# Kernel optimization log

Measured on AMD Instinct MI355X. Metric: run time of the kernel, lower is better.

## Reference

```python
import jax, jax.numpy as jnp
import numpy as np


def setup_inputs() -> dict:
    key = jax.random.key(0)
    kx, kw, kt, ks, kd, km = jax.random.split(key, 6)
    B, N, E, H, D = 1, 100000, 3200000, 8, 64
    X = jax.random.normal(kx, (B, N, H, D), dtype=jnp.float32)
    # glorot_uniform-like init for [D, H, 1]
    limit = (6.0 / (D + H)) ** 0.5
    attn_kernel = jax.random.uniform(kw, (D, H, 1), dtype=jnp.float32, minval=-limit, maxval=limit)
    targets = jax.random.randint(kt, (B, E), 0, N)
    sources = jax.random.randint(ks, (B, E), 0, N)
    degree = jax.random.uniform(kd, (B, N), dtype=jnp.float32)
    # tf.nn.dropout(x, 0.5): keep w.p. 0.5, scale kept by 1/0.5 = 2
    drop_mask = (jax.random.uniform(km, (B, E, H)) < 0.5).astype(jnp.float32) * 2.0
    return {"X": X, "attn_kernel": attn_kernel, "targets": targets,
            "sources": sources, "degree": degree, "drop_mask": drop_mask, "N": N}


def reference(X, attn_kernel, targets, sources, degree, drop_mask, N):
    # X: [B, N, H, D]; attn_kernel: [D, H, 1]; targets/sources: [B, E]
    B, _, H, D = X.shape
    E = targets.shape[1]
    W = attn_kernel[:, :, 0]                          # [D, H]
    attn = jnp.einsum('bnhd,dh->bnh', X, W)           # per-node scalar per head
    # gather to edges (tf.gather batch_dims=1): [B, E, H]
    e = jnp.take_along_axis(attn, sources[..., None], axis=1)
    e = jnp.tanh(e)
    # TF unsorted_segment_max with rank-2 ids pools over (batch, edge) jointly
    ids = targets.reshape(B * E)
    ef = e.reshape(B * E, H)
    m = jax.ops.segment_max(ef, ids, num_segments=N)  # [N, H]
    ef = jnp.exp(ef - m[ids])
    s = jax.ops.segment_max(ef, ids, num_segments=N) + 1e-9  # NOTE: max, not sum (faithful)
    ef = ef / s[ids]
    out = ef.reshape(B, E, H) * drop_mask
    return out[..., None]                             # [B, E, H, 1]
```

## Files before the change

kernel.cpp:

```cpp
#include <hip/hip_runtime.h>
#include <stdint.h>

#define HD 8
#define DD 64

typedef float  vf4 __attribute__((ext_vector_type(4)));
typedef unsigned vu4 __attribute__((ext_vector_type(4)));

__device__ __forceinline__ unsigned fmap(float f) {
    unsigned u = __float_as_uint(f);
    return u ^ (unsigned)(((int)u >> 31) | 0x80000000);
}
__device__ __forceinline__ float funmap(unsigned u) {
    u ^= ((int)u < 0) ? 0x80000000u : 0xFFFFFFFFu;
    return __uint_as_float(u);
}
#define FMAP_NEG_INF 0x007FFFFFu

__device__ __forceinline__ unsigned pack_bf16_rne(float a, float b) {
    unsigned ua = __float_as_uint(a); ua += 0x7FFF + ((ua >> 16) & 1);
    unsigned ub = __float_as_uint(b); ub += 0x7FFF + ((ub >> 16) & 1);
    return (ua >> 16) | (ub & 0xFFFF0000u);
}
__device__ __forceinline__ float bf_lo(unsigned u) { return __uint_as_float(u << 16); }
__device__ __forceinline__ float bf_hi(unsigned u) { return __uint_as_float(u & 0xFFFF0000u); }

__global__ __launch_bounds__(256) void attn_tanh_kernel(
    const float* __restrict__ X, const float* __restrict__ Wk,
    unsigned* __restrict__ t_pk, uint2* __restrict__ m_init, int N)
{
    __shared__ float Ws[DD * HD];
    int tid = threadIdx.x;
    for (int i = tid; i < DD * HD; i += 256) Ws[i] = Wk[i];
    __syncthreads();

    int wave = tid >> 6, lane = tid & 63;
    int n0 = (blockIdx.x * 4 + wave) * 2;
    if (n0 >= N) return;
    bool two = (n0 + 1 < N);

    const vf4* Xa = (const vf4*)X + (size_t)n0 * 128;
    vf4 z = {0.f, 0.f, 0.f, 0.f};
    vf4 xv0 = __builtin_nontemporal_load(Xa + lane);
    vf4 xv1 = __builtin_nontemporal_load(Xa + 64 + lane);
    vf4 xv2 = two ? __builtin_nontemporal_load(Xa + 128 + lane) : z;
    vf4 xv3 = two ? __builtin_nontemporal_load(Xa + 192 + lane) : z;

    int h0 = lane >> 4, d0 = (lane & 15) << 2;
    int h1 = 4 + h0;
    float w00 = Ws[(d0 + 0) * HD + h0], w01 = Ws[(d0 + 1) * HD + h0],
          w02 = Ws[(d0 + 2) * HD + h0], w03 = Ws[(d0 + 3) * HD + h0];
    float w10 = Ws[(d0 + 0) * HD + h1], w11 = Ws[(d0 + 1) * HD + h1],
          w12 = Ws[(d0 + 2) * HD + h1], w13 = Ws[(d0 + 3) * HD + h1];

    float p0 = xv0.x * w00 + xv0.y * w01 + xv0.z * w02 + xv0.w * w03;
    float p1 = xv1.x * w10 + xv1.y * w11 + xv1.z * w12 + xv1.w * w13;
    float p2 = xv2.x * w00 + xv2.y * w01 + xv2.z * w02 + xv2.w * w03;
    float p3 = xv3.x * w10 + xv3.y * w11 + xv3.z * w12 + xv3.w * w13;

    for (int off = 8; off; off >>= 1) {
        p0 += __shfl_xor(p0, off);
        p1 += __shfl_xor(p1, off);
        p2 += __shfl_xor(p2, off);
        p3 += __shfl_xor(p3, off);
    }
    if ((lane & 15) == 0) {
        int g = lane >> 4;
        t_pk[(size_t)n0 * 4 + g] = pack_bf16_rne(tanhf(p0), tanhf(p1));
        m_init[(size_t)n0 * 4 + g] = make_uint2(FMAP_NEG_INF, FMAP_NEG_INF);
        if (two) {
            t_pk[(size_t)(n0 + 1) * 4 + g] = pack_bf16_rne(tanhf(p2), tanhf(p3));
            m_init[(size_t)(n0 + 1) * 4 + g] = make_uint2(FMAP_NEG_INF, FMAP_NEG_INF);
        }
    }
}

__global__ __launch_bounds__(256) void seg_max_kernel(
    const int* __restrict__ sources, const int* __restrict__ targets,
    const uint4* __restrict__ t_pk4, unsigned* __restrict__ m_u, int E)
{
    int e = blockIdx.x * 256 + threadIdx.x;
    if (e >= E) return;
    int s  = __builtin_nontemporal_load(sources + e);
    int tg = __builtin_nontemporal_load(targets + e);
    uint4 tv = t_pk4[s];
    unsigned* mp = m_u + (size_t)tg * HD;
    const uint4* m4 = (const uint4*)mp;
    uint4 c0 = m4[0];
    uint4 c1 = m4[1];
    unsigned f;
    f = fmap(bf_lo(tv.x)); if (f > c0.x) atomicMax(mp + 0, f);
    f = fmap(bf_hi(tv.x)); if (f > c0.y) atomicMax(mp + 1, f);
    f = fmap(bf_lo(tv.y)); if (f > c0.z) atomicMax(mp + 2, f);
    f = fmap(bf_hi(tv.y)); if (f > c0.w) atomicMax(mp + 3, f);
    f = fmap(bf_lo(tv.z)); if (f > c1.x) atomicMax(mp + 4, f);
    f = fmap(bf_hi(tv.z)); if (f > c1.y) atomicMax(mp + 5, f);
    f = fmap(bf_lo(tv.w)); if (f > c1.z) atomicMax(mp + 6, f);
    f = fmap(bf_hi(tv.w)); if (f > c1.w) atomicMax(mp + 7, f);
}

__global__ __launch_bounds__(256) void pack_m_kernel(
    const unsigned* __restrict__ m_u, uint4* __restrict__ m_pk, int N)
{
    int n = blockIdx.x * 256 + threadIdx.x;
    if (n >= N) return;
    const uint4* mu4 = (const uint4*)m_u + (size_t)n * 2;
    uint4 c0 = mu4[0];
    uint4 c1 = mu4[1];
    uint4 o;
    o.x = (__float_as_uint(funmap(c0.x)) >> 16) | (__float_as_uint(funmap(c0.y)) & 0xFFFF0000u);
    o.y = (__float_as_uint(funmap(c0.z)) >> 16) | (__float_as_uint(funmap(c0.w)) & 0xFFFF0000u);
    o.z = (__float_as_uint(funmap(c1.x)) >> 16) | (__float_as_uint(funmap(c1.y)) & 0xFFFF0000u);
    o.w = (__float_as_uint(funmap(c1.z)) >> 16) | (__float_as_uint(funmap(c1.w)) & 0xFFFF0000u);
    m_pk[n] = o;
}

__global__ __launch_bounds__(256) void finalize_kernel(
    const int* __restrict__ sources, const int* __restrict__ targets,
    const uint4* __restrict__ t_pk4, const uint4* __restrict__ m_pk,
    const float* __restrict__ dm, float* __restrict__ out, int E)
{
    int e = blockIdx.x * 256 + threadIdx.x;
    if (e >= E) return;
    int s  = __builtin_nontemporal_load(sources + e);
    int tg = __builtin_nontemporal_load(targets + e);
    uint4 tv = t_pk4[s];
    uint4 mv = m_pk[tg];
    const vf4* dm4 = (const vf4*)dm;
    vf4 d0 = __builtin_nontemporal_load(dm4 + (size_t)e * 2);
    vf4 d1 = __builtin_nontemporal_load(dm4 + (size_t)e * 2 + 1);
    vf4 o0, o1;
    o0.x = expf(bf_lo(tv.x) - bf_lo(mv.x)) * d0.x;
    o0.y = expf(bf_lo(tv.y) - bf_lo(mv.y)) * d0.y;
    o0.z = expf(bf_lo(tv.z) - bf_lo(mv.z)) * d0.z;
    o0.w = expf(bf_lo(tv.w) - bf_lo(mv.w)) * d0.w;
    o1.x = expf(bf_hi(tv.x) - bf_hi(mv.x)) * d1.x;
    o1.y = expf(bf_hi(tv.y) - bf_hi(mv.y)) * d1.y;
    o1.z = expf(bf_hi(tv.z) - bf_hi(mv.z)) * d1.z;
    o1.w = expf(bf_hi(tv.w) - bf_hi(mv.w)) * d1.w;
    vf4* out4 = (vf4*)out;
    __builtin_nontemporal_store(o0, out4 + (size_t)e * 2);
    __builtin_nontemporal_store(o1, out4 + (size_t)e * 2 + 1);
}

extern "C" void kernel_launch(void* const* d_in, const int* in_sizes, int n_in,
                              void* d_out, int out_size, void* d_ws, size_t ws_size,
                              hipStream_t stream)
{
    const float* X       = (const float*)d_in[0];
    const float* Wk      = (const float*)d_in[1];
    const int*   targets = (const int*)d_in[2];
    const int*   sources = (const int*)d_in[3];
    const float* dm      = (const float*)d_in[5];

    int E = in_sizes[2];
    int N = in_sizes[4];

    unsigned* t_pk = (unsigned*)d_ws;
    unsigned* m_u  = (unsigned*)d_ws + (size_t)N * 4;
    uint4*    m_pk = (uint4*)((unsigned*)d_ws + (size_t)N * 12);

    float* out = (float*)d_out;

    int blocksA = (N + 7) / 8;
    attn_tanh_kernel<<<blocksA, 256, 0, stream>>>(X, Wk, t_pk, (uint2*)m_u, N);

    int blocksE = (E + 255) / 256;
    seg_max_kernel<<<blocksE, 256, 0, stream>>>(sources, targets, (const uint4*)t_pk, m_u, E);

    int blocksN = (N + 255) / 256;
    pack_m_kernel<<<blocksN, 256, 0, stream>>>(m_u, m_pk, N);

    finalize_kernel<<<blocksE, 256, 0, stream>>>(sources, targets, (const uint4*)t_pk, m_pk, dm, out, E);
}
```

Before: 640.9 us.

## Replace per-edge atomicMax segment-max with bucketed edge lists and wave reduction

Per-edge segment max is restructured so each edge does one atomicAdd on a per-target counter and stores its source index into a fixed-capacity per-target bucket. Edges past the bucket capacity fall back to atomicMax. A new per-node kernel reduces each bucket with one wave using shuffles and writes packed bf16 maxima, replacing the pack kernel. This trades up to eight contended atomics per edge for one atomicAdd plus a scattered index write, but adds a large list buffer and an extra gather pass over t_pk. Counter zeroing is folded into the attention kernel, and the old path stays as a fallback when workspace is too small.

```diff
diff --git a/kernel.cpp b/kernel.cpp
--- a/kernel.cpp
+++ b/kernel.cpp
@@ -3,9 +3,9 @@
 
 #define HD 8
 #define DD 64
+#define CAP 64
 
 typedef float  vf4 __attribute__((ext_vector_type(4)));
-typedef unsigned vu4 __attribute__((ext_vector_type(4)));
 
 __device__ __forceinline__ unsigned fmap(float f) {
     unsigned u = __float_as_uint(f);
@@ -27,11 +27,16 @@
 
 __global__ __launch_bounds__(256) void attn_tanh_kernel(
     const float* __restrict__ X, const float* __restrict__ Wk,
-    unsigned* __restrict__ t_pk, uint2* __restrict__ m_init, int N)
+    unsigned* __restrict__ t_pk, uint2* __restrict__ m_init,
+    unsigned* __restrict__ cnt, int N)
 {
     __shared__ float Ws[DD * HD];
     int tid = threadIdx.x;
     for (int i = tid; i < DD * HD; i += 256) Ws[i] = Wk[i];
+
+    int gid = blockIdx.x * 256 + tid;
+    if (cnt != nullptr && gid < N) cnt[gid] = 0;
+
     __syncthreads();
 
     int wave = tid >> 6, lane = tid & 63;
@@ -74,6 +79,84 @@
         }
     }
 }
+
+__global__ __launch_bounds__(256) void scatter_kernel(
+    const int* __restrict__ sources, const int* __restrict__ targets,
+    unsigned* __restrict__ cnt, unsigned* __restrict__ lst,
+    const uint4* __restrict__ t_pk4, unsigned* __restrict__ m_u, int E)
+{
+    int e = blockIdx.x * 256 + threadIdx.x;
+    if (e >= E) return;
+    int s  = __builtin_nontemporal_load(sources + e);
+    int tg = __builtin_nontemporal_load(targets + e);
+    unsigned pos = atomicAdd(cnt + tg, 1u);
+    if (pos < CAP) {
+        lst[(size_t)tg * CAP + pos] = (unsigned)s;
+    } else {
+        uint4 tv = t_pk4[s];
+        unsigned* mp = m_u + (size_t)tg * HD;
+        atomicMax(mp + 0, fmap(bf_lo(tv.x)));
+        atomicMax(mp + 1, fmap(bf_hi(tv.x)));
+        atomicMax(mp + 2, fmap(bf_lo(tv.y)));
+        atomicMax(mp + 3, fmap(bf_hi(tv.y)));
+        atomicMax(mp + 4, fmap(bf_lo(tv.z)));
+        atomicMax(mp + 5, fmap(bf_hi(tv.z)));
+        atomicMax(mp + 6, fmap(bf_lo(tv.w)));
+        atomicMax(mp + 7, fmap(bf_hi(tv.w)));
+    }
+}
+
+__global__ __launch_bounds__(256) void gather_max_kernel(
+    const unsigned* __restrict__ cnt, const unsigned* __restrict__ lst,
+    const uint4* __restrict__ t_pk4, const unsigned* __restrict__ m_u,
+    uint4* __restrict__ m_pk, int N)
+{
+    int wave = threadIdx.x >> 6, lane = threadIdx.x & 63;
+    int n = blockIdx.x * 4 + wave;
+    if (n >= N) return;
+
+    unsigned c = cnt[n];
+    if (c > CAP) c = CAP;
+
+    float v0 = -INFINITY, v1 = -INFINITY, v2 = -INFINITY, v3 = -INFINITY,
+          v4 = -INFINITY, v5 = -INFINITY, v6 = -INFINITY, v7 = -INFINITY;
+    if ((unsigned)lane < c) {
+        unsigned s = lst[(size_t)n * CAP + lane];
+        uint4 tv = t_pk4[s];
+        v0 = bf_lo(tv.x); v1 = bf_hi(tv.x);
+        v2 = bf_lo(tv.y); v3 = bf_hi(tv.y);
+        v4 = bf_lo(tv.z); v5 = bf_hi(tv.z);
+        v6 = bf_lo(tv.w); v7 = bf_hi(tv.w);
+    }
+    for (int off = 32; off; off >>= 1) {
+        v0 = fmaxf(v0, __shfl_xor(v0, off));
+        v1 = fmaxf(v1, __shfl_xor(v1, off));
+        v2 = fmaxf(v2, __shfl_xor(v2, off));
+        v3 = fmaxf(v3, __shfl_xor(v3, off));
+        v4 = fmaxf(v4, __shfl_xor(v4, off));
+        v5 = fmaxf(v5, __shfl_xor(v5, off));
+        v6 = fmaxf(v6, __shfl_xor(v6, off));
+        v7 = fmaxf(v7, __shfl_xor(v7, off));
+    }
+    if (lane == 0) {
+        const unsigned* mu = m_u + (size_t)n * HD;
+        v0 = fmaxf(v0, funmap(mu[0]));
+        v1 = fmaxf(v1, funmap(mu[1]));
+        v2 = fmaxf(v2, funmap(mu[2]));
+        v3 = fmaxf(v3, funmap(mu[3]));
+        v4 = fmaxf(v4, funmap(mu[4]));
+        v5 = fmaxf(v5, funmap(mu[5]));
+        v6 = fmaxf(v6, funmap(mu[6]));
+        v7 = fmaxf(v7, funmap(mu[7]));
+        uint4 o;
+        o.x = pack_bf16_rne(v0, v1);
+        o.y = pack_bf16_rne(v2, v3);
+        o.z = pack_bf16_rne(v4, v5);
+        o.w = pack_bf16_rne(v6, v7);
+        m_pk[n] = o;
+    }
+}
+
 
 __global__ __launch_bounds__(256) void seg_max_kernel(
     const int* __restrict__ sources, const int* __restrict__ targets,
@@ -156,20 +239,35 @@
     int E = in_sizes[2];
     int N = in_sizes[4];
 
-    unsigned* t_pk = (unsigned*)d_ws;
-    unsigned* m_u  = (unsigned*)d_ws + (size_t)N * 4;
-    uint4*    m_pk = (uint4*)((unsigned*)d_ws + (size_t)N * 12);
-
     float* out = (float*)d_out;
-
     int blocksA = (N + 7) / 8;
-    attn_tanh_kernel<<<blocksA, 256, 0, stream>>>(X, Wk, t_pk, (uint2*)m_u, N);
-
     int blocksE = (E + 255) / 256;
-    seg_max_kernel<<<blocksE, 256, 0, stream>>>(sources, targets, (const uint4*)t_pk, m_u, E);
-
-    int blocksN = (N + 255) / 256;
-    pack_m_kernel<<<blocksN, 256, 0, stream>>>(m_u, m_pk, N);
-
-    finalize_kernel<<<blocksE, 256, 0, stream>>>(sources, targets, (const uint4*)t_pk, m_pk, dm, out, E);
-}
+
+    size_t needed = (size_t)N * 324;
+
+    char* w = (char*)d_ws;
+    unsigned* t_pk = (unsigned*)w;
+    unsigned* m_u  = (unsigned*)(w + (size_t)N * 16);
+    uint4*    m_pk = (uint4*)  (w + (size_t)N * 48);
+
+    if (ws_size >= needed) {
+        unsigned* cnt = (unsigned*)(w + (size_t)N * 64);
+        unsigned* lst = (unsigned*)(w + (size_t)N * 68);
+
+        attn_tanh_kernel<<<blocksA, 256, 0, stream>>>(X, Wk, t_pk, (uint2*)m_u, cnt, N);
+        scatter_kernel<<<blocksE, 256, 0, stream>>>(sources, targets, cnt, lst,
+                                                    (const uint4*)t_pk, m_u, E);
+        int blocksG = (N + 3) / 4;
+        gather_max_kernel<<<blocksG, 256, 0, stream>>>(cnt, lst, (const uint4*)t_pk,
+                                                       m_u, m_pk, N);
+        finalize_kernel<<<blocksE, 256, 0, stream>>>(sources, targets, (const uint4*)t_pk,
+                                                     m_pk, dm, out, E);
+    } else {
+        attn_tanh_kernel<<<blocksA, 256, 0, stream>>>(X, Wk, t_pk, (uint2*)m_u, nullptr, N);
+        seg_max_kernel<<<blocksE, 256, 0, stream>>>(sources, targets, (const uint4*)t_pk, m_u, E);
+        int blocksN = (N + 255) / 256;
+        pack_m_kernel<<<blocksN, 256, 0, stream>>>(m_u, m_pk, N);
+        finalize_kernel<<<blocksE, 256, 0, stream>>>(sources, targets, (const uint4*)t_pk,
+                                                     m_pk, dm, out, E);
+    }
+}
```

Measured after the change: 705.3 us. 10.0% more time.

## Bin edges by target range and reduce segment max in shared memory

Applied to the files above, without the earlier changes.

Replaces the global atomicMax segment-max with a two-pass scheme. Edges are first binned by target block of 512 nodes into per-bin workspace buffers, each packed as (local target, source). Then one block per bin reduces with shared-memory atomics and writes the packed bf16 max directly, which removes the separate pack kernel. Overflow edges fall back to global atomics. The change also drops the nontemporal load and store hints, and it adds an extra pass over the edge arrays plus buffer writes and reads.

```diff
diff --git a/kernel.cpp b/kernel.cpp
--- a/kernel.cpp
+++ b/kernel.cpp
@@ -3,9 +3,11 @@
 
 #define HD 8
 #define DD 64
+#define BSHIFT 9
+#define BRANGE 512
+#define NBMAX 256
 
 typedef float  vf4 __attribute__((ext_vector_type(4)));
-typedef unsigned vu4 __attribute__((ext_vector_type(4)));
 
 __device__ __forceinline__ unsigned fmap(float f) {
     unsigned u = __float_as_uint(f);
@@ -27,11 +29,16 @@
 
 __global__ __launch_bounds__(256) void attn_tanh_kernel(
     const float* __restrict__ X, const float* __restrict__ Wk,
-    unsigned* __restrict__ t_pk, uint2* __restrict__ m_init, int N)
+    unsigned* __restrict__ t_pk, uint2* __restrict__ m_init,
+    unsigned* __restrict__ gcnt, int NB, int N)
 {
     __shared__ float Ws[DD * HD];
     int tid = threadIdx.x;
     for (int i = tid; i < DD * HD; i += 256) Ws[i] = Wk[i];
+
+    int gid = blockIdx.x * 256 + tid;
+    if (gcnt != nullptr && gid < NB) gcnt[gid] = 0;
+
     __syncthreads();
 
     int wave = tid >> 6, lane = tid & 63;
@@ -41,10 +48,10 @@
 
     const vf4* Xa = (const vf4*)X + (size_t)n0 * 128;
     vf4 z = {0.f, 0.f, 0.f, 0.f};
-    vf4 xv0 = __builtin_nontemporal_load(Xa + lane);
-    vf4 xv1 = __builtin_nontemporal_load(Xa + 64 + lane);
-    vf4 xv2 = two ? __builtin_nontemporal_load(Xa + 128 + lane) : z;
-    vf4 xv3 = two ? __builtin_nontemporal_load(Xa + 192 + lane) : z;
+    vf4 xv0 = Xa[lane];
+    vf4 xv1 = Xa[64 + lane];
+    vf4 xv2 = two ? Xa[128 + lane] : z;
+    vf4 xv3 = two ? Xa[192 + lane] : z;
 
     int h0 = lane >> 4, d0 = (lane & 15) << 2;
     int h1 = 4 + h0;
@@ -74,6 +81,118 @@
         }
     }
 }
+
+__global__ __launch_bounds__(256) void bin_kernel(
+    const int* __restrict__ sources, const int* __restrict__ targets,
+    unsigned* __restrict__ gcnt, unsigned* __restrict__ buf,
+    const uint4* __restrict__ t_pk4, unsigned* __restrict__ m_u,
+    int NB, int CAPB, int SRC_BITS, int E)
+{
+    __shared__ unsigned hist[NBMAX];
+    __shared__ unsigned base[NBMAX];
+    __shared__ unsigned cur[NBMAX];
+    int tid = threadIdx.x;
+    if (tid < NB) { hist[tid] = 0; cur[tid] = 0; }
+    __syncthreads();
+
+    int e0 = blockIdx.x * 4096;
+    #pragma unroll
+    for (int k = 0; k < 16; ++k) {
+        int e = e0 + k * 256 + tid;
+        if (e < E) {
+            int tg = targets[e];
+            atomicAdd(&hist[tg >> BSHIFT], 1u);
+        }
+    }
+    __syncthreads();
+    if (tid < NB && hist[tid] != 0)
+        base[tid] = atomicAdd(gcnt + tid, hist[tid]);
+    __syncthreads();
+
+    #pragma unroll
+    for (int k = 0; k < 16; ++k) {
+        int e = e0 + k * 256 + tid;
+        if (e < E) {
+            int tg = targets[e];
+            int s  = sources[e];
+            int b  = tg >> BSHIFT;
+            unsigned pos = base[b] + atomicAdd(&cur[b], 1u);
+            if (pos < (unsigned)CAPB) {
+                buf[(size_t)b * CAPB + pos] =
+                    ((unsigned)(tg & (BRANGE - 1)) << SRC_BITS) | (unsigned)s;
+            } else {
+                uint4 tv = t_pk4[s];
+                unsigned* mp = m_u + (size_t)tg * HD;
+                atomicMax(mp + 0, fmap(bf_lo(tv.x)));
+                atomicMax(mp + 1, fmap(bf_hi(tv.x)));
+                atomicMax(mp + 2, fmap(bf_lo(tv.y)));
+                atomicMax(mp + 3, fmap(bf_hi(tv.y)));
+                atomicMax(mp + 4, fmap(bf_lo(tv.z)));
+                atomicMax(mp + 5, fmap(bf_hi(tv.z)));
+                atomicMax(mp + 6, fmap(bf_lo(tv.w)));
+                atomicMax(mp + 7, fmap(bf_hi(tv.w)));
+            }
+        }
+    }
+}
+
+__global__ __launch_bounds__(256) void reduce_kernel(
+    const unsigned* __restrict__ gcnt, const unsigned* __restrict__ buf,
+    const uint4* __restrict__ t_pk4, const unsigned* __restrict__ m_u,
+    uint4* __restrict__ m_pk, int CAPB, int SRC_BITS, int N)
+{
+    __shared__ unsigned mt[BRANGE * HD];
+    int tid = threadIdx.x;
+    int b = blockIdx.x;
+    for (int i = tid; i < BRANGE * HD; i += 256) mt[i] = FMAP_NEG_INF;
+    __syncthreads();
+
+    unsigned cnt = gcnt[b];
+    if (cnt > (unsigned)CAPB) cnt = CAPB;
+    unsigned srcmask = (1u << SRC_BITS) - 1;
+    const unsigned* bb = buf + (size_t)b * CAPB;
+
+    for (unsigned i = tid; i < cnt; i += 256) {
+        unsigned rec = bb[i];
+        unsigned s  = rec & srcmask;
+        unsigned tl = rec >> SRC_BITS;
+        uint4 tv = t_pk4[s];
+        unsigned* mp = mt + tl * HD;
+        atomicMax(mp + 0, fmap(bf_lo(tv.x)));
+        atomicMax(mp + 1, fmap(bf_hi(tv.x)));
+        atomicMax(mp + 2, fmap(bf_lo(tv.y)));
+        atomicMax(mp + 3, fmap(bf_hi(tv.y)));
+        atomicMax(mp + 4, fmap(bf_lo(tv.z)));
+        atomicMax(mp + 5, fmap(bf_hi(tv.z)));
+        atomicMax(mp + 6, fmap(bf_lo(tv.w)));
+        atomicMax(mp + 7, fmap(bf_hi(tv.w)));
+    }
+    __syncthreads();
+
+    int n0 = b << BSHIFT;
+    for (int tl = tid; tl < BRANGE; tl += 256) {
+        int n = n0 + tl;
+        if (n < N) {
+            const unsigned* ms = mt + tl * HD;
+            const unsigned* mu = m_u + (size_t)n * HD;
+            float v0 = fmaxf(funmap(ms[0]), funmap(mu[0]));
+            float v1 = fmaxf(funmap(ms[1]), funmap(mu[1]));
+            float v2 = fmaxf(funmap(ms[2]), funmap(mu[2]));
+            float v3 = fmaxf(funmap(ms[3]), funmap(mu[3]));
+            float v4 = fmaxf(funmap(ms[4]), funmap(mu[4]));
+            float v5 = fmaxf(funmap(ms[5]), funmap(mu[5]));
+            float v6 = fmaxf(funmap(ms[6]), funmap(mu[6]));
+            float v7 = fmaxf(funmap(ms[7]), funmap(mu[7]));
+            uint4 o;
+            o.x = pack_bf16_rne(v0, v1);
+            o.y = pack_bf16_rne(v2, v3);
+            o.z = pack_bf16_rne(v4, v5);
+            o.w = pack_bf16_rne(v6, v7);
+            m_pk[n] = o;
+        }
+    }
+}
+
 
 __global__ __launch_bounds__(256) void seg_max_kernel(
     const int* __restrict__ sources, const int* __restrict__ targets,
@@ -127,8 +246,8 @@
     uint4 tv = t_pk4[s];
     uint4 mv = m_pk[tg];
     const vf4* dm4 = (const vf4*)dm;
-    vf4 d0 = __builtin_nontemporal_load(dm4 + (size_t)e * 2);
-    vf4 d1 = __builtin_nontemporal_load(dm4 + (size_t)e * 2 + 1);
+    vf4 d0 = dm4[(size_t)e * 2];
+    vf4 d1 = dm4[(size_t)e * 2 + 1];
     vf4 o0, o1;
     o0.x = expf(bf_lo(tv.x) - bf_lo(mv.x)) * d0.x;
     o0.y = expf(bf_lo(tv.y) - bf_lo(mv.y)) * d0.y;
@@ -139,8 +258,8 @@
     o1.z = expf(bf_hi(tv.z) - bf_hi(mv.z)) * d1.z;
     o1.w = expf(bf_hi(tv.w) - bf_hi(mv.w)) * d1.w;
     vf4* out4 = (vf4*)out;
-    __builtin_nontemporal_store(o0, out4 + (size_t)e * 2);
-    __builtin_nontemporal_store(o1, out4 + (size_t)e * 2 + 1);
+    out4[(size_t)e * 2]     = o0;
+    out4[(size_t)e * 2 + 1] = o1;
 }
 
 extern "C" void kernel_launch(void* const* d_in, const int* in_sizes, int n_in,
@@ -156,20 +275,44 @@
     int E = in_sizes[2];
     int N = in_sizes[4];
 
-    unsigned* t_pk = (unsigned*)d_ws;
-    unsigned* m_u  = (unsigned*)d_ws + (size_t)N * 4;
-    uint4*    m_pk = (uint4*)((unsigned*)d_ws + (size_t)N * 12);
-
     float* out = (float*)d_out;
-
     int blocksA = (N + 7) / 8;
-    attn_tanh_kernel<<<blocksA, 256, 0, stream>>>(X, Wk, t_pk, (uint2*)m_u, N);
-
     int blocksE = (E + 255) / 256;
-    seg_max_kernel<<<blocksE, 256, 0, stream>>>(sources, targets, (const uint4*)t_pk, m_u, E);
-
-    int blocksN = (N + 255) / 256;
-    pack_m_kernel<<<blocksN, 256, 0, stream>>>(m_u, m_pk, N);
-
-    finalize_kernel<<<blocksE, 256, 0, stream>>>(sources, targets, (const uint4*)t_pk, m_pk, dm, out, E);
-}
+
+    int NB = (N + BRANGE - 1) >> BSHIFT;
+    int SRC_BITS = 1;
+    while ((1 << SRC_BITS) < N && SRC_BITS < 31) ++SRC_BITS;
+    bool packable = (NB <= NBMAX) && (SRC_BITS + BSHIFT <= 32);
+    long long capll = ((long long)(E + NB - 1) / (NB > 0 ? NB : 1));
+    capll = (capll * 3) / 2;
+    capll = (capll + 255) & ~255LL;
+    int CAPB = (int)capll;
+
+    size_t needed = (size_t)N * 68 + (size_t)NB * (size_t)CAPB * 4;
+
+    char* w = (char*)d_ws;
+    unsigned* t_pk = (unsigned*)w;
+    unsigned* m_u  = (unsigned*)(w + (size_t)N * 16);
+    uint4*    m_pk = (uint4*)  (w + (size_t)N * 48);
+
+    if (packable && ws_size >= needed) {
+        unsigned* gcnt = (unsigned*)(w + (size_t)N * 64);
+        unsigned* buf  = (unsigned*)(w + (size_t)N * 68);
+
+        attn_tanh_kernel<<<blocksA, 256, 0, stream>>>(X, Wk, t_pk, (uint2*)m_u, gcnt, NB, N);
+        int blocksB = (E + 4095) / 4096;
+        bin_kernel<<<blocksB, 256, 0, stream>>>(sources, targets, gcnt, buf,
+                                                (const uint4*)t_pk, m_u, NB, CAPB, SRC_BITS, E);
+        reduce_kernel<<<NB, 256, 0, stream>>>(gcnt, buf, (const uint4*)t_pk, m_u,
+                                              m_pk, CAPB, SRC_BITS, N);
+        finalize_kernel<<<blocksE, 256, 0, stream>>>(sources, targets, (const uint4*)t_pk,
+                                                     m_pk, dm, out, E);
+    } else {
+        attn_tanh_kernel<<<blocksA, 256, 0, stream>>>(X, Wk, t_pk, (uint2*)m_u, nullptr, 0, N);
+        seg_max_kernel<<<blocksE, 256, 0, stream>>>(sources, targets, (const uint4*)t_pk, m_u, E);
+        int blocksN = (N + 255) / 256;
+        pack_m_kernel<<<blocksN, 256, 0, stream>>>(m_u, m_pk, N);
+        finalize_kernel<<<blocksE, 256, 0, stream>>>(sources, targets, (const uint4*)t_pk,
+                                                     m_pk, dm, out, E);
+    }
+}
```

Result: faster. 530.5 us (-17.2%).
